# Kernel tuning notes

Hardware: AMD Instinct MI355X
Metric: run time of the kernel (lower is better)

Reference implementation:

```python
import jax, jax.numpy as jnp
import numpy as np

B, N, D = 32, 2048, 768
DEPTH, HEADS, GRID, NC = 12, 12, 10, 40
T = GRID * GRID + 1          # 100 pillars + cls token
HD = D // HEADS
SCALE = HD ** -0.5
INTERVAL = 0.2
MLP_H = 4 * D
EPS = 1e-5


def setup_inputs() -> dict:
    key = jax.random.key(0)
    ks = list(jax.random.split(key, 12))
    n = lambda k, s, std: (jax.random.normal(k, s, dtype=jnp.float32) * std)
    return {
        "x": jax.random.uniform(ks[0], (B, N, 3), minval=-1.0, maxval=1.0, dtype=jnp.float32),
        "W1": n(ks[1], (6, 32), 0.1),
        "W2": n(ks[2], (32, 64), 0.1),
        "W3": n(ks[3], (64, 128), 0.1),
        "Wa": n(ks[4], (256, D), 0.05),
        "bn_g": jnp.ones((GRID * GRID,), jnp.float32),
        "bn_b": jnp.zeros((GRID * GRID,), jnp.float32),
        "bn_mean": jnp.zeros((GRID * GRID,), jnp.float32),
        "bn_var": jnp.ones((GRID * GRID,), jnp.float32),
        "cls_token": jnp.zeros((1, 1, D), jnp.float32),
        "pos_embed": n(ks[5], (1, T, D), 0.02),
        "ln1_g": jnp.ones((DEPTH, D), jnp.float32), "ln1_b": jnp.zeros((DEPTH, D), jnp.float32),
        "qkv_w": n(ks[6], (DEPTH, D, 3 * D), 0.01),
        "proj_w": n(ks[7], (DEPTH, D, D), 0.01), "proj_b": jnp.zeros((DEPTH, D), jnp.float32),
        "ln2_g": jnp.ones((DEPTH, D), jnp.float32), "ln2_b": jnp.zeros((DEPTH, D), jnp.float32),
        "fc1_w": n(ks[8], (DEPTH, D, MLP_H), 0.01), "fc1_b": jnp.zeros((DEPTH, MLP_H), jnp.float32),
        "fc2_w": n(ks[9], (DEPTH, MLP_H, D), 0.01), "fc2_b": jnp.zeros((DEPTH, D), jnp.float32),
        "norm_g": jnp.ones((D,), jnp.float32), "norm_b": jnp.zeros((D,), jnp.float32),
        "head_w": n(ks[10], (D, NC), 0.01), "head_b": jnp.zeros((NC,), jnp.float32),
    }


def _layer_norm(x, g, b):
    m = jnp.mean(x, -1, keepdims=True)
    v = jnp.mean(jnp.square(x - m), -1, keepdims=True)
    return (x - m) * jax.lax.rsqrt(v + EPS) * g + b


def reference(x, W1, W2, W3, Wa, bn_g, bn_b, bn_mean, bn_var, cls_token, pos_embed,
              ln1_g, ln1_b, qkv_w, proj_w, proj_b, ln2_g, ln2_b,
              fc1_w, fc1_b, fc2_w, fc2_b, norm_g, norm_b, head_w, head_b):
    # ---- Pillar encoder (voxel bucketing via segment ops) ----
    # torch code reorders columns (y,z,x)->(z,y,x); voxel index uses (y,x)
    p = x[..., jnp.array([1, 0, 2])]                     # [B,N,3] = (z,y,x)
    yx = jnp.clip(p[..., 1:] + 1.0, 0.0, 1.99)
    idx = jnp.floor(yx / INTERVAL).astype(jnp.int32)     # [B,N,2] in [0,GRID)
    cell = (idx[..., 0] * GRID + idx[..., 1]
            + jnp.arange(B, dtype=jnp.int32)[:, None] * GRID * GRID).reshape(-1)
    pf = p.reshape(-1, 3)                                # [B*N,3]
    S = B * GRID * GRID
    cnt = jax.ops.segment_sum(jnp.ones((B * N,), pf.dtype), cell, num_segments=S)
    centroid = jax.ops.segment_sum(pf, cell, num_segments=S) / jnp.maximum(cnt, 1.0)[:, None]
    aug = jnp.concatenate([pf, pf - centroid[cell]], -1)  # [B*N,6]
    h = jax.nn.relu(aug @ W1)
    h = jax.nn.relu(h @ W2)
    h = jax.nn.relu(h @ W3)                               # [B*N,128]
    pooled = jax.ops.segment_max(h, cell, num_segments=S)  # per-pillar max
    h2 = jax.nn.relu(jnp.concatenate([h, pooled[cell]], -1) @ Wa)  # [B*N,768]
    pillar = jax.ops.segment_max(h2, cell, num_segments=S)
    pillar = jnp.where(cnt[:, None] > 0, pillar, 0.0)     # empty cells stay zero
    seq = pillar.reshape(B, GRID * GRID, D)               # flatten order = y*GRID+x
    # BatchNorm1d(100) over the sequence-position channel (eval mode)
    inv = bn_g * jax.lax.rsqrt(bn_var + EPS)
    seq = (seq - bn_mean[None, :, None]) * inv[None, :, None] + bn_b[None, :, None]

    # ---- ViT stack ----
    tokens = jnp.concatenate([jnp.broadcast_to(cls_token, (B, 1, D)), seq], 1) + pos_embed

    def block(hh, prm):
        g1, b1, qw, pw, pb, g2, b2, f1w, f1b, f2w, f2b = prm
        y = _layer_norm(hh, g1, b1)
        qkv = (y @ qw).reshape(B, T, 3, HEADS, HD)
        q, k, v = qkv[:, :, 0], qkv[:, :, 1], qkv[:, :, 2]   # [B,T,H,hd]
        attn = jax.nn.softmax(jnp.einsum('bqhd,bkhd->bhqk', q, k) * SCALE, -1)
        o = jnp.einsum('bhqk,bkhd->bqhd', attn, v).reshape(B, T, D)
        hh = hh + o @ pw + pb
        y = _layer_norm(hh, g2, b2)
        y = jax.nn.gelu(y @ f1w + f1b, approximate=False)
        hh = hh + y @ f2w + f2b
        return hh, None

    prms = (ln1_g, ln1_b, qkv_w, proj_w, proj_b, ln2_g, ln2_b, fc1_w, fc1_b, fc2_w, fc2_b)
    tokens, _ = jax.lax.scan(block, tokens, prms)
    out = _layer_norm(tokens, norm_g, norm_b)[:, 0] @ head_w + head_b  # cls head
    return out
```

## Files before the change

kernel.cpp:

```cpp
#include <hip/hip_runtime.h>

typedef __bf16 bf8 __attribute__((ext_vector_type(8)));
typedef float  f4  __attribute__((ext_vector_type(4)));
typedef unsigned long long uptr;

__device__ __forceinline__ void gload16(const void* g, void* l){
  __builtin_amdgcn_global_load_lds(
      (const __attribute__((address_space(1))) unsigned int*)(uptr)g,
      (__attribute__((address_space(3))) unsigned int*)(uptr)l,
      16, 0, 0);
}


__global__ __launch_bounds__(256) void k_cell(const float* __restrict__ x, int* __restrict__ cellArr,
                                              float* __restrict__ cnt, float* __restrict__ cent){
  int p = blockIdx.x*256 + threadIdx.x;
  float x0 = x[p*3+0], x1 = x[p*3+1], x2 = x[p*3+2];
  float y0 = fminf(fmaxf(x0 + 1.0f, 0.0f), 1.99f);
  float y1 = fminf(fmaxf(x2 + 1.0f, 0.0f), 1.99f);
  int i0 = (int)floorf(y0 / 0.2f);
  int i1 = (int)floorf(y1 / 0.2f);
  int b = p >> 11;
  int cell = b*100 + i0*10 + i1;
  cellArr[p] = cell;
  atomicAdd(&cnt[cell], 1.0f);
  atomicAdd(&cent[cell*3+0], x1);
  atomicAdd(&cent[cell*3+1], x0);
  atomicAdd(&cent[cell*3+2], x2);
}

__global__ __launch_bounds__(256) void k_scan(const float* __restrict__ cnt,
                                              int* __restrict__ base, int* __restrict__ wptr){
  __shared__ int a[256];
  int tid = threadIdx.x;
  int start = tid*13, end = start+13; if (end > 3200) end = 3200;
  int local = 0;
  for (int i = start; i < end; i++) local += (int)cnt[i];
  a[tid] = local;
  __syncthreads();
  for (int off = 1; off < 256; off <<= 1){
    int t = (tid >= off) ? a[tid - off] : 0;
    __syncthreads();
    a[tid] += t;
    __syncthreads();
  }
  int run = a[tid] - local;
  for (int i = start; i < end; i++){
    base[i] = run; wptr[i] = run;
    run += (int)cnt[i];
  }
}

__global__ __launch_bounds__(256) void k_scatter(const int* __restrict__ cellArr,
                                                 int* __restrict__ wptr, int* __restrict__ order){
  int p = blockIdx.x*256 + threadIdx.x;
  int c = cellArr[p];
  int pos = atomicAdd(&wptr[c], 1);
  order[pos] = p;
}

__global__ __launch_bounds__(256) void k_pointmlp(const float* __restrict__ x,
    const float* __restrict__ W1, const float* __restrict__ W2, const float* __restrict__ W3,
    const float* __restrict__ cent, const float* __restrict__ cnt, const int* __restrict__ cellArr,
    const int* __restrict__ order, int* __restrict__ cellSlot, __bf16* __restrict__ A2){
  __shared__ float w1s[6*32];
  __shared__ float w2s[32*64];
  __shared__ float w3s[64*128];
  int tid = threadIdx.x;
  for (int i = tid; i < 192;  i += 256) w1s[i] = W1[i];
  for (int i = tid; i < 2048; i += 256) w2s[i] = W2[i];
  for (int i = tid; i < 8192; i += 256) w3s[i] = W3[i];
  __syncthreads();
  int s = blockIdx.x*256 + tid;
  int p = order[s];
  int cell = cellArr[p];
  cellSlot[s] = cell;
  float pf0 = x[p*3+1], pf1 = x[p*3+0], pf2 = x[p*3+2];
  float cc = fmaxf(cnt[cell], 1.0f);
  float a[6] = {pf0, pf1, pf2,
                pf0 - cent[cell*3+0]/cc, pf1 - cent[cell*3+1]/cc, pf2 - cent[cell*3+2]/cc};
  float h1[32];
  #pragma unroll
  for (int f = 0; f < 32; f++){
    float t = 0.f;
    #pragma unroll
    for (int i = 0; i < 6; i++) t += a[i]*w1s[i*32+f];
    h1[f] = fmaxf(t, 0.f);
  }
  float h2[64];
  #pragma unroll
  for (int f = 0; f < 64; f++){
    float t = 0.f;
    #pragma unroll
    for (int i = 0; i < 32; i++) t += h1[i]*w2s[i*64+f];
    h2[f] = fmaxf(t, 0.f);
  }
  for (int f0 = 0; f0 < 128; f0 += 8){
    __bf16 tmp[8];
    #pragma unroll
    for (int j = 0; j < 8; j++){
      float t = 0.f;
      #pragma unroll
      for (int i = 0; i < 64; i++) t += h2[i]*w3s[i*128+f0+j];
      tmp[j] = (__bf16)fmaxf(t, 0.f);
    }
    *reinterpret_cast<uint4*>(&A2[(size_t)s*256 + f0]) = *reinterpret_cast<uint4*>(tmp);
  }
}

__global__ __launch_bounds__(128) void k_poolh(const __bf16* __restrict__ A2,
    const int* __restrict__ base, const float* __restrict__ cnt, float* __restrict__ pooled){
  int c = blockIdx.x, f = threadIdx.x;
  int b0 = base[c], n = (int)cnt[c];
  float v = 0.f;
  for (int k = 0; k < n; k++) v = fmaxf(v, (float)A2[(size_t)(b0+k)*256 + f]);
  pooled[c*128 + f] = v;
}

__global__ __launch_bounds__(256) void k_fill(const float* __restrict__ pooled,
    const int* __restrict__ cellSlot, __bf16* __restrict__ A2){
  int idx = blockIdx.x*256 + threadIdx.x;
  int s = idx >> 4, f0 = (idx & 15) << 3;
  int cell = cellSlot[s];
  const float* pp = &pooled[cell*128 + f0];
  __bf16 tmp[8];
  #pragma unroll
  for (int j = 0; j < 8; j++) tmp[j] = (__bf16)pp[j];
  *reinterpret_cast<uint4*>(&A2[(size_t)s*256 + 128 + f0]) = *reinterpret_cast<uint4*>(tmp);
}

__global__ __launch_bounds__(256) void k_pillarpool(const __bf16* __restrict__ h2c,
    const int* __restrict__ base, const float* __restrict__ cnt, float* __restrict__ pillar, int cs){
  int c = blockIdx.x, tid = threadIdx.x;
  int b0 = base[c], e0 = b0 + (int)cnt[c];
  int lo = b0 > cs ? b0 : cs;
  int hi = e0 < cs + 16384 ? e0 : cs + 16384;
  if (lo >= hi) return;
  for (int f = tid; f < 768; f += 256){
    float v = 0.f;
    for (int s = lo; s < hi; s++) v = fmaxf(v, (float)h2c[(size_t)(s - cs)*768 + f]);
    atomicMax((int*)&pillar[(size_t)c*768 + f], __float_as_int(v));
  }
}

__global__ void k_assemble(const float* __restrict__ pillar,
    const float* __restrict__ bn_g, const float* __restrict__ bn_b,
    const float* __restrict__ bn_mean, const float* __restrict__ bn_var,
    const float* __restrict__ cls_t, const float* __restrict__ pos,
    float* __restrict__ tokens){
  int idx = blockIdx.x*256 + threadIdx.x;
  int m = idx / 768, d = idx % 768;
  int b = m / 101, t = m % 101;
  float v;
  if (t == 0) v = cls_t[d];
  else {
    int s = t - 1;
    float pv = pillar[((size_t)b*100 + s)*768 + d];
    float inv = bn_g[s]*rsqrtf(bn_var[s] + 1e-5f);
    v = (pv - bn_mean[s])*inv + bn_b[s];
  }
  tokens[idx] = v + pos[t*768 + d];
}


__global__ __launch_bounds__(256) void k_transpose(const float* __restrict__ W, __bf16* __restrict__ Wt,
                                                   int K, int N){
  __shared__ float t[32][33];
  int n0 = blockIdx.x*32, k0 = blockIdx.y*32;
  int tx = threadIdx.x & 31, ty = threadIdx.x >> 5;
  #pragma unroll
  for (int i = 0; i < 32; i += 8){
    int k = k0 + ty + i, n = n0 + tx;
    t[ty+i][tx] = (k < K && n < N) ? W[(size_t)k*N + n] : 0.f;
  }
  __syncthreads();
  #pragma unroll
  for (int i = 0; i < 32; i += 8){
    int n = n0 + ty + i, k = k0 + tx;
    if (n < N && k < K) Wt[(size_t)n*K + k] = (__bf16)t[tx][ty+i];
  }
}

__global__ __launch_bounds__(256) void k_transpose_all(
    const float* __restrict__ qw, const float* __restrict__ pw,
    const float* __restrict__ f1, const float* __restrict__ f2,
    __bf16* __restrict__ wq, __bf16* __restrict__ wp,
    __bf16* __restrict__ w1, __bf16* __restrict__ w2){
  int id = blockIdx.x;
  size_t l = blockIdx.y;
  const float* W; __bf16* Wt; int K, N, nx, ny;
  if (id < 1728){ W=qw+l*768*2304; Wt=wq+l*768*2304; K=768;  N=2304; nx=id%72; ny=id/72; }
  else if (id < 2304){ id-=1728; W=pw+l*768*768;  Wt=wp+l*768*768;  K=768;  N=768;  nx=id%24; ny=id/24; }
  else if (id < 4608){ id-=2304; W=f1+l*768*3072; Wt=w1+l*768*3072; K=768;  N=3072; nx=id%96; ny=id/96; }
  else {               id-=4608; W=f2+l*3072*768; Wt=w2+l*3072*768; K=3072; N=768;  nx=id%24; ny=id/24; }
  __shared__ float t[32][33];
  int n0 = nx*32, k0 = ny*32;
  int tx = threadIdx.x & 31, ty = threadIdx.x >> 5;
  #pragma unroll
  for (int i = 0; i < 32; i += 8) t[ty+i][tx] = W[(size_t)(k0+ty+i)*N + n0+tx];
  __syncthreads();
  #pragma unroll
  for (int i = 0; i < 32; i += 8) Wt[(size_t)(n0+ty+i)*K + k0+tx] = (__bf16)t[tx][ty+i];
}


__global__ __launch_bounds__(256) void k_gemm(const __bf16* __restrict__ A, const __bf16* __restrict__ Bt,
    const float* __restrict__ bias, const float* __restrict__ res,
    float* __restrict__ outF, __bf16* __restrict__ outB,
    int M, int N, int K, int act, int splitK){
  __shared__ alignas(16) __bf16 As[128*64];
  __shared__ alignas(16) __bf16 Bs[128*64];
  int tid  = threadIdx.x;
  int m0 = blockIdx.y*128, n0 = blockIdx.x*128;
  int z = blockIdx.z;
  int kLen = K / splitK, k0 = z*kLen;
  int wave = tid >> 6, lane = tid & 63;
  int wm = (wave >> 1)*64, wn = (wave & 1)*64;
  int r16 = lane & 15, q = lane >> 4;
  int srow = tid >> 3;
  int sslot = tid & 7;
  int slotX[2];
  #pragma unroll
  for (int kk = 0; kk < 2; kk++) slotX[kk] = ((kk*4 + q) ^ (r16 & 7)) * 8;
  f4 acc[4][4];
  #pragma unroll
  for (int i = 0; i < 4; i++)
    #pragma unroll
    for (int j = 0; j < 4; j++) acc[i][j] = (f4){0.f,0.f,0.f,0.f};

  for (int kt = k0; kt < k0 + kLen; kt += 64){
    #pragma unroll
    for (int rr = 0; rr < 4; rr++){
      int row = rr*32 + srow;
      int scol = kt + ((sslot ^ (row & 7)) * 8);
      int gm = m0 + row; if (gm >= M) gm = M - 1;
      gload16(A  + (size_t)gm*K + scol, (char*)As + rr*4096 + tid*16);
      int gn = n0 + row;
      gload16(Bt + (size_t)gn*K + scol, (char*)Bs + rr*4096 + tid*16);
    }
    __syncthreads();
    #pragma unroll
    for (int kk = 0; kk < 2; kk++){
      bf8 af[4], bq[4];
      #pragma unroll
      for (int i = 0; i < 4; i++) af[i] = *reinterpret_cast<const bf8*>(&As[(wm + i*16 + r16)*64 + slotX[kk]]);
      #pragma unroll
      for (int j = 0; j < 4; j++) bq[j] = *reinterpret_cast<const bf8*>(&Bs[(wn + j*16 + r16)*64 + slotX[kk]]);
      #pragma unroll
      for (int i = 0; i < 4; i++)
        #pragma unroll
        for (int j = 0; j < 4; j++)
          acc[i][j] = __builtin_amdgcn_mfma_f32_16x16x32_bf16(af[i], bq[j], acc[i][j], 0, 0, 0);
    }
    __syncthreads();
  }

  #pragma unroll
  for (int i = 0; i < 4; i++){
    #pragma unroll
    for (int j = 0; j < 4; j++){
      int nn = n0 + wn + j*16 + r16;
      float bv = (bias && z == 0) ? bias[nn] : 0.f;
      #pragma unroll
      for (int r = 0; r < 4; r++){
        int m = m0 + wm + i*16 + q*4 + r;
        if (m >= M) continue;
        float v = acc[i][j][r] + bv;
        if (splitK > 1){
          atomicAdd(&outF[(size_t)m*N + nn], v);
        } else {
          if (act == 1) v = fmaxf(v, 0.f);
          else if (act == 2) v = 0.5f*v*(1.f + erff(v*0.70710678118654752f));
          if (outB){
            outB[(size_t)m*N + nn] = (__bf16)v;
          } else {
            float rv = res ? res[(size_t)m*N + nn] : 0.f;
            outF[(size_t)m*N + nn] = rv + v;
          }
        }
      }
    }
  }
}


__global__ __launch_bounds__(256) void k_ln(const float* __restrict__ in, const float* __restrict__ g,
    const float* __restrict__ bta, __bf16* __restrict__ outB, float* __restrict__ outF, int rowMul){
  int orow = blockIdx.x;
  const float* xr = in + (size_t)orow*rowMul*768;
  int tid = threadIdx.x;
  float v0 = xr[tid], v1 = xr[tid+256], v2 = xr[tid+512];
  float s = v0+v1+v2, s2 = v0*v0 + v1*v1 + v2*v2;
  #pragma unroll
  for (int off = 32; off > 0; off >>= 1){ s += __shfl_xor(s, off); s2 += __shfl_xor(s2, off); }
  __shared__ float rs[4], rq[4];
  int w = tid >> 6;
  if ((tid & 63) == 0){ rs[w] = s; rq[w] = s2; }
  __syncthreads();
  s = rs[0]+rs[1]+rs[2]+rs[3]; s2 = rq[0]+rq[1]+rq[2]+rq[3];
  float mean = s*(1.f/768.f);
  float var  = s2*(1.f/768.f) - mean*mean;
  float rstd = rsqrtf(var + 1e-5f);
  size_t ob = (size_t)orow*768;
  float y0 = (v0-mean)*rstd*g[tid]     + bta[tid];
  float y1 = (v1-mean)*rstd*g[tid+256] + bta[tid+256];
  float y2 = (v2-mean)*rstd*g[tid+512] + bta[tid+512];
  if (outB){ outB[ob+tid]=(__bf16)y0; outB[ob+tid+256]=(__bf16)y1; outB[ob+tid+512]=(__bf16)y2; }
  else     { outF[ob+tid]=y0;         outF[ob+tid+256]=y1;         outF[ob+tid+512]=y2; }
}


#define PSS 136
#define VTS 136

__global__ __launch_bounds__(256, 3) void k_attn(const __bf16* __restrict__ qkvB, __bf16* __restrict__ o){
  __shared__ alignas(16) __bf16 smem[64*VTS + 64*PSS];
  __bf16* Vt = smem;
  __bf16* Ps = smem + 64*VTS;
  int bh = blockIdx.x >> 1, half = blockIdx.x & 1;
  int b = bh / 12, h = bh % 12;
  int tid = threadIdx.x;
  const __bf16* basep = qkvB + (size_t)(b*101)*2304 + h*64;

  #pragma unroll
  for (int it = 0; it < 4; it++){
    int c = tid + it*256;
    int t = c >> 3, d0 = c & 7;
    bf8 v;
    if (t < 101){
      v = *reinterpret_cast<const bf8*>(&basep[(size_t)t*2304 + 1536 + d0*8]);
    } else {
      #pragma unroll
      for (int j = 0; j < 8; j++) v[j] = (__bf16)0.f;
    }
    #pragma unroll
    for (int j = 0; j < 8; j++){
      int jj = (j + d0) & 7;
      Vt[(d0*8 + jj)*VTS + t] = v[jj];
    }
  }

  int wave = tid >> 6, lane = tid & 63;
  int r16 = lane & 15, q = lane >> 4;
  int m0 = half*64 + wave*16;

  f4 sacc[7];
  #pragma unroll
  for (int j = 0; j < 7; j++) sacc[j] = (f4){0.f,0.f,0.f,0.f};
  #pragma unroll
  for (int kt = 0; kt < 64; kt += 32){
    int row = m0 + r16; if (row > 100) row = 100;
    bf8 aq = *reinterpret_cast<const bf8*>(&basep[(size_t)row*2304 + kt + q*8]);
    #pragma unroll
    for (int j = 0; j < 7; j++){
      int krow = j*16 + r16; if (krow > 100) krow = 100;
      bf8 kf = *reinterpret_cast<const bf8*>(&basep[(size_t)krow*2304 + 768 + kt + q*8]);
      sacc[j] = __builtin_amdgcn_mfma_f32_16x16x32_bf16(aq, kf, sacc[j], 0, 0, 0);
    }
  }

  #pragma unroll
  for (int r = 0; r < 4; r++){
    float s[7];
    #pragma unroll
    for (int j = 0; j < 7; j++){
      s[j] = sacc[j][r] * 0.125f;
      if (j == 6 && r16 >= 5) s[j] = -1e30f;
    }
    float mx = s[0];
    #pragma unroll
    for (int j = 1; j < 7; j++) mx = fmaxf(mx, s[j]);
    #pragma unroll
    for (int off2 = 1; off2 < 16; off2 <<= 1) mx = fmaxf(mx, __shfl_xor(mx, off2));
    float p[7], sum = 0.f;
    #pragma unroll
    for (int j = 0; j < 7; j++){ p[j] = __expf(s[j] - mx); sum += p[j]; }
    #pragma unroll
    for (int off2 = 1; off2 < 16; off2 <<= 1) sum += __shfl_xor(sum, off2);
    float inv = 1.f / sum;
    int lr = wave*16 + q*4 + r;
    #pragma unroll
    for (int j = 0; j < 7; j++) Ps[lr*PSS + j*16 + r16] = (__bf16)(p[j]*inv);
    Ps[lr*PSS + 112 + r16] = (__bf16)0.f;
  }
  __syncthreads();

  f4 oacc[4];
  #pragma unroll
  for (int n = 0; n < 4; n++) oacc[n] = (f4){0.f,0.f,0.f,0.f};
  #pragma unroll
  for (int kt = 0; kt < 128; kt += 32){
    bf8 af = *reinterpret_cast<const bf8*>(&Ps[(wave*16 + r16)*PSS + kt + q*8]);
    #pragma unroll
    for (int n = 0; n < 4; n++){
      bf8 bq = *reinterpret_cast<const bf8*>(&Vt[(n*16 + r16)*VTS + kt + q*8]);
      oacc[n] = __builtin_amdgcn_mfma_f32_16x16x32_bf16(af, bq, oacc[n], 0, 0, 0);
    }
  }

  #pragma unroll
  for (int n = 0; n < 4; n++){
    #pragma unroll
    for (int r = 0; r < 4; r++){
      int t = m0 + q*4 + r;
      if (t < 101)
        o[((size_t)(b*101 + t))*768 + h*64 + n*16 + r16] = (__bf16)oacc[n][r];
    }
  }
}

__global__ void k_head(const float* __restrict__ cls, const float* __restrict__ hw,
                       const float* __restrict__ hb, float* __restrict__ out){
  int b = blockIdx.x, c = threadIdx.x;
  if (c < 40){
    float s = hb[c];
    for (int k = 0; k < 768; k++) s += cls[b*768 + k]*hw[k*40 + c];
    out[b*40 + c] = s;
  }
}


extern "C" void kernel_launch(void* const* d_in, const int* in_sizes, int n_in,
                              void* d_out, int out_size, void* d_ws, size_t ws_size,
                              hipStream_t stream){
  const float* x       = (const float*)d_in[0];
  const float* W1      = (const float*)d_in[1];
  const float* W2      = (const float*)d_in[2];
  const float* W3      = (const float*)d_in[3];
  const float* Wa      = (const float*)d_in[4];
  const float* bn_g    = (const float*)d_in[5];
  const float* bn_b    = (const float*)d_in[6];
  const float* bn_mean = (const float*)d_in[7];
  const float* bn_var  = (const float*)d_in[8];
  const float* cls_t   = (const float*)d_in[9];
  const float* pos     = (const float*)d_in[10];
  const float* ln1_g   = (const float*)d_in[11];
  const float* ln1_b   = (const float*)d_in[12];
  const float* qkv_w   = (const float*)d_in[13];
  const float* proj_w  = (const float*)d_in[14];
  const float* proj_b  = (const float*)d_in[15];
  const float* ln2_g   = (const float*)d_in[16];
  const float* ln2_b   = (const float*)d_in[17];
  const float* fc1_w   = (const float*)d_in[18];
  const float* fc1_b   = (const float*)d_in[19];
  const float* fc2_w   = (const float*)d_in[20];
  const float* fc2_b   = (const float*)d_in[21];
  const float* norm_g  = (const float*)d_in[22];
  const float* norm_b  = (const float*)d_in[23];
  const float* head_w  = (const float*)d_in[24];
  const float* head_b  = (const float*)d_in[25];

  char* ws = (char*)d_ws;
  size_t off = 0;
  auto alloc = [&](size_t bytes)->void*{ void* p = ws + off; off += (bytes + 255) & ~(size_t)255; return p; };
  float* cnt     = (float*)alloc(3200*4);
  float* cent    = (float*)alloc(3200*3*4);
  float* pillar  = (float*)alloc((size_t)3200*768*4);
  size_t zbytes  = (size_t)((char*)pillar - (char*)cnt) + (size_t)3200*768*4;
  int*   base    = (int*)  alloc(3200*4);
  int*   wptr    = (int*)  alloc(3200*4);
  int*   order   = (int*)  alloc((size_t)65536*4);
  int*   cellSlot= (int*)  alloc((size_t)65536*4);
  int*   cellArr = (int*)  alloc((size_t)65536*4);
  float* pooled  = (float*)alloc((size_t)3200*128*4);
  float* tokens  = (float*)alloc((size_t)3232*768*4);
  float* cls     = (float*)alloc((size_t)32*768*4);
  __bf16* wWa    = (__bf16*)alloc((size_t)768*256*2);
  __bf16* wq12   = (__bf16*)alloc((size_t)12*768*2304*2);
  __bf16* wp12   = (__bf16*)alloc((size_t)12*768*768*2);
  __bf16* w112   = (__bf16*)alloc((size_t)12*768*3072*2);
  __bf16* w212   = (__bf16*)alloc((size_t)12*3072*768*2);
  size_t offR = off;
  __bf16* A2  = (__bf16*)alloc((size_t)65536*256*2);
  __bf16* h2c = (__bf16*)alloc((size_t)16384*768*2);
  size_t endPillarPhase = off;
  off = offR;
  __bf16* y    = (__bf16*)alloc((size_t)3232*768*2);
  __bf16* qkvB = (__bf16*)alloc((size_t)3232*2304*2);
  __bf16* o    = (__bf16*)alloc((size_t)3232*768*2);
  __bf16* mlp  = (__bf16*)alloc((size_t)3232*3072*2);
  if (off < endPillarPhase) off = endPillarPhase;
  (void)ws_size; (void)in_sizes; (void)n_in; (void)out_size;

  hipMemsetAsync(cnt, 0, zbytes, stream);

  k_transpose_all<<<dim3(6912,12),256,0,stream>>>(qkv_w, proj_w, fc1_w, fc2_w, wq12, wp12, w112, w212);
  k_transpose<<<dim3(24,8),256,0,stream>>>(Wa, wWa, 256, 768);

  k_cell<<<256,256,0,stream>>>(x, cellArr, cnt, cent);
  k_scan<<<1,256,0,stream>>>(cnt, base, wptr);
  k_scatter<<<256,256,0,stream>>>(cellArr, wptr, order);
  k_pointmlp<<<256,256,0,stream>>>(x, W1, W2, W3, cent, cnt, cellArr, order, cellSlot, A2);
  k_poolh<<<3200,128,0,stream>>>(A2, base, cnt, pooled);
  k_fill<<<4096,256,0,stream>>>(pooled, cellSlot, A2);
  for (int c = 0; c < 4; c++){
    k_gemm<<<dim3(6,128),256,0,stream>>>(A2 + (size_t)c*16384*256, wWa, nullptr, nullptr,
                                         nullptr, h2c, 16384, 768, 256, 1, 1);
    k_pillarpool<<<3200,256,0,stream>>>(h2c, base, cnt, pillar, c*16384);
  }
  k_assemble<<<9696,256,0,stream>>>(pillar, bn_g, bn_b, bn_mean, bn_var, cls_t, pos, tokens);

  for (int l = 0; l < 12; l++){
    __bf16* wq = wq12 + (size_t)l*768*2304;
    __bf16* wp = wp12 + (size_t)l*768*768;
    __bf16* w1 = w112 + (size_t)l*768*3072;
    __bf16* w2 = w212 + (size_t)l*3072*768;
    k_ln<<<3232,256,0,stream>>>(tokens, ln1_g + l*768, ln1_b + l*768, y, nullptr, 1);
    k_gemm<<<dim3(18,26),256,0,stream>>>(y, wq, nullptr, nullptr, nullptr, qkvB, 3232, 2304, 768, 0, 1);
    k_attn<<<768,256,0,stream>>>(qkvB, o);
    k_gemm<<<dim3(6,26,4),256,0,stream>>>(o, wp, proj_b + l*768, nullptr, tokens, nullptr,
                                          3232, 768, 768, 0, 4);
    k_ln<<<3232,256,0,stream>>>(tokens, ln2_g + l*768, ln2_b + l*768, y, nullptr, 1);
    k_gemm<<<dim3(24,26),256,0,stream>>>(y, w1, fc1_b + l*3072, nullptr, nullptr, mlp, 3232, 3072, 768, 2, 1);
    k_gemm<<<dim3(6,26,4),256,0,stream>>>(mlp, w2, fc2_b + l*768, nullptr, tokens, nullptr,
                                          3232, 768, 3072, 0, 4);
  }

  k_ln<<<32,256,0,stream>>>(tokens, norm_g, norm_b, nullptr, cls, 101);
  k_head<<<32,64,0,stream>>>(cls, head_w, head_b, (float*)d_out);
}
```

Before: 2.906 ms.

## Merge pillar GEMM chunks, vectorize weight transpose, parallelize head

The four chunked pillar GEMM plus pool launches become one GEMM over all 65536 rows, followed by a single pool pass that writes results directly instead of using atomicMax. The weight transpose kernel now uses float4 loads, bf16 shared tiles of 128x32 and 16-byte stores, so it needs four times fewer blocks. The head kernel splits the K reduction across 6 thread groups using shared memory. The h2c buffer grows fourfold, which raises workspace use and the memory traffic of the pillar phase.

```diff
diff --git a/kernel.cpp b/kernel.cpp
--- a/kernel.cpp
+++ b/kernel.cpp
@@ -130,16 +130,14 @@
 }
 
 __global__ __launch_bounds__(256) void k_pillarpool(const __bf16* __restrict__ h2c,
-    const int* __restrict__ base, const float* __restrict__ cnt, float* __restrict__ pillar, int cs){
+    const int* __restrict__ base, const float* __restrict__ cnt, float* __restrict__ pillar){
   int c = blockIdx.x, tid = threadIdx.x;
-  int b0 = base[c], e0 = b0 + (int)cnt[c];
-  int lo = b0 > cs ? b0 : cs;
-  int hi = e0 < cs + 16384 ? e0 : cs + 16384;
-  if (lo >= hi) return;
+  int b0 = base[c], n = (int)cnt[c];
+  if (n == 0) return;
   for (int f = tid; f < 768; f += 256){
     float v = 0.f;
-    for (int s = lo; s < hi; s++) v = fmaxf(v, (float)h2c[(size_t)(s - cs)*768 + f]);
-    atomicMax((int*)&pillar[(size_t)c*768 + f], __float_as_int(v));
+    for (int s = b0; s < b0 + n; s++) v = fmaxf(v, (float)h2c[(size_t)s*768 + f]);
+    pillar[(size_t)c*768 + f] = v;
   }
 }
 
@@ -188,19 +186,29 @@
     __bf16* __restrict__ w1, __bf16* __restrict__ w2){
   int id = blockIdx.x;
   size_t l = blockIdx.y;
-  const float* W; __bf16* Wt; int K, N, nx, ny;
-  if (id < 1728){ W=qw+l*768*2304; Wt=wq+l*768*2304; K=768;  N=2304; nx=id%72; ny=id/72; }
-  else if (id < 2304){ id-=1728; W=pw+l*768*768;  Wt=wp+l*768*768;  K=768;  N=768;  nx=id%24; ny=id/24; }
-  else if (id < 4608){ id-=2304; W=f1+l*768*3072; Wt=w1+l*768*3072; K=768;  N=3072; nx=id%96; ny=id/96; }
-  else {               id-=4608; W=f2+l*3072*768; Wt=w2+l*3072*768; K=3072; N=768;  nx=id%24; ny=id/24; }
-  __shared__ float t[32][33];
-  int n0 = nx*32, k0 = ny*32;
-  int tx = threadIdx.x & 31, ty = threadIdx.x >> 5;
-  #pragma unroll
-  for (int i = 0; i < 32; i += 8) t[ty+i][tx] = W[(size_t)(k0+ty+i)*N + n0+tx];
-  __syncthreads();
-  #pragma unroll
-  for (int i = 0; i < 32; i += 8) Wt[(size_t)(n0+ty+i)*K + k0+tx] = (__bf16)t[tx][ty+i];
+  const float* W; __bf16* Wt; int K, N, kx, nx;
+  if (id < 432){               W=qw+l*768*2304; Wt=wq+l*768*2304; K=768;  N=2304; kx=id%6;  nx=id/6; }
+  else if (id < 576){ id-=432; W=pw+l*768*768;  Wt=wp+l*768*768;  K=768;  N=768;  kx=id%6;  nx=id/6; }
+  else if (id < 1152){ id-=576;  W=f1+l*768*3072; Wt=w1+l*768*3072; K=768;  N=3072; kx=id%6;  nx=id/6; }
+  else {               id-=1152; W=f2+l*3072*768; Wt=w2+l*3072*768; K=3072; N=768;  kx=id%24; nx=id/24; }
+  __shared__ __bf16 t[32][136];
+  int k0 = kx*128, n0 = nx*32;
+  int tid = threadIdx.x;
+  int kr = tid >> 3, nc = (tid & 7)*4;
+  #pragma unroll
+  for (int i = 0; i < 4; i++){
+    int k = kr + i*32;
+    float4 v = *reinterpret_cast<const float4*>(&W[(size_t)(k0+k)*N + n0 + nc]);
+    t[nc+0][k] = (__bf16)v.x; t[nc+1][k] = (__bf16)v.y;
+    t[nc+2][k] = (__bf16)v.z; t[nc+3][k] = (__bf16)v.w;
+  }
+  __syncthreads();
+  int nr = tid >> 4, ks = (tid & 15)*8;
+  #pragma unroll
+  for (int j = 0; j < 2; j++){
+    int n = j*16 + nr;
+    *reinterpret_cast<uint4*>(&Wt[(size_t)(n0+n)*K + k0 + ks]) = *reinterpret_cast<uint4*>(&t[n][ks]);
+  }
 }
 
 
@@ -409,13 +417,23 @@
   }
 }
 
-__global__ void k_head(const float* __restrict__ cls, const float* __restrict__ hw,
+__global__ __launch_bounds__(256) void k_head(const float* __restrict__ cls, const float* __restrict__ hw,
                        const float* __restrict__ hb, float* __restrict__ out){
-  int b = blockIdx.x, c = threadIdx.x;
-  if (c < 40){
-    float s = hb[c];
-    for (int k = 0; k < 768; k++) s += cls[b*768 + k]*hw[k*40 + c];
-    out[b*40 + c] = s;
+  int b = blockIdx.x;
+  int tid = threadIdx.x;
+  int c = tid % 40, s = tid / 40;
+  __shared__ float part[6][40];
+  if (s < 6){
+    float acc = 0.f;
+    for (int k = s*128; k < s*128 + 128; k++) acc += cls[b*768 + k]*hw[k*40 + c];
+    part[s][c] = acc;
+  }
+  __syncthreads();
+  if (tid < 40){
+    float v = hb[tid];
+    #pragma unroll
+    for (int i = 0; i < 6; i++) v += part[i][tid];
+    out[b*40 + tid] = v;
   }
 }
 
@@ -472,7 +490,7 @@
   __bf16* w212   = (__bf16*)alloc((size_t)12*3072*768*2);
   size_t offR = off;
   __bf16* A2  = (__bf16*)alloc((size_t)65536*256*2);
-  __bf16* h2c = (__bf16*)alloc((size_t)16384*768*2);
+  __bf16* h2c = (__bf16*)alloc((size_t)65536*768*2);
   size_t endPillarPhase = off;
   off = offR;
   __bf16* y    = (__bf16*)alloc((size_t)3232*768*2);
@@ -484,7 +502,7 @@
 
   hipMemsetAsync(cnt, 0, zbytes, stream);
 
-  k_transpose_all<<<dim3(6912,12),256,0,stream>>>(qkv_w, proj_w, fc1_w, fc2_w, wq12, wp12, w112, w212);
+  k_transpose_all<<<dim3(1728,12),256,0,stream>>>(qkv_w, proj_w, fc1_w, fc2_w, wq12, wp12, w112, w212);
   k_transpose<<<dim3(24,8),256,0,stream>>>(Wa, wWa, 256, 768);
 
   k_cell<<<256,256,0,stream>>>(x, cellArr, cnt, cent);
@@ -493,11 +511,8 @@
   k_pointmlp<<<256,256,0,stream>>>(x, W1, W2, W3, cent, cnt, cellArr, order, cellSlot, A2);
   k_poolh<<<3200,128,0,stream>>>(A2, base, cnt, pooled);
   k_fill<<<4096,256,0,stream>>>(pooled, cellSlot, A2);
-  for (int c = 0; c < 4; c++){
-    k_gemm<<<dim3(6,128),256,0,stream>>>(A2 + (size_t)c*16384*256, wWa, nullptr, nullptr,
-                                         nullptr, h2c, 16384, 768, 256, 1, 1);
-    k_pillarpool<<<3200,256,0,stream>>>(h2c, base, cnt, pillar, c*16384);
-  }
+  k_gemm<<<dim3(6,512),256,0,stream>>>(A2, wWa, nullptr, nullptr, nullptr, h2c, 65536, 768, 256, 1, 1);
+  k_pillarpool<<<3200,256,0,stream>>>(h2c, base, cnt, pillar);
   k_assemble<<<9696,256,0,stream>>>(pillar, bn_g, bn_b, bn_mean, bn_var, cls_t, pos, tokens);
 
   for (int l = 0; l < 12; l++){
@@ -517,5 +532,5 @@
   }
 
   k_ln<<<32,256,0,stream>>>(tokens, norm_g, norm_b, nullptr, cls, 101);
-  k_head<<<32,64,0,stream>>>(cls, head_w, head_b, (float*)d_out);
-}
+  k_head<<<32,256,0,stream>>>(cls, head_w, head_b, (float*)d_out);
+}
```

After: 2.832 ms. 2.5% less time.
